# Kernel tuning notes

Measured on AMD Instinct MI355X. Metric: run time of the kernel, lower is better.

The kernel has to match this reference:

```python
import jax, jax.numpy as jnp
import numpy as np

B, N, H, E = 64, 512, 32, 4
N_STEPS = 5
ANNO = 1


def setup_inputs() -> dict:
    key = jax.random.key(0)
    ks = jax.random.split(key, 20)
    sc_h = 1.0 / np.sqrt(H)
    sc_3h = 1.0 / np.sqrt(3 * H)
    sc_ha = 1.0 / np.sqrt(H + ANNO)
    inp = {
        "x": jax.random.normal(ks[0], (B, N, H), jnp.float32),
        "a": jax.random.uniform(ks[1], (B, N, ANNO), jnp.float32),
        "m": jax.random.uniform(ks[2], (B, N, 2 * N * E), jnp.float32),
        # fc_in / fc_out: hidden -> hidden*n_edge (torch Linear: W [out,in])
        "W_in": jax.random.normal(ks[3], (H * E, H), jnp.float32) * sc_h,
        "b_in": jax.random.normal(ks[4], (H * E,), jnp.float32) * sc_h,
        "W_out": jax.random.normal(ks[5], (H * E, H), jnp.float32) * sc_h,
        "b_out": jax.random.normal(ks[6], (H * E,), jnp.float32) * sc_h,
        # GRU-style gates: 3*hidden -> hidden
        "Wz": jax.random.normal(ks[7], (H, 3 * H), jnp.float32) * sc_3h,
        "bz": jax.random.normal(ks[8], (H,), jnp.float32) * sc_3h,
        "Wr": jax.random.normal(ks[9], (H, 3 * H), jnp.float32) * sc_3h,
        "br": jax.random.normal(ks[10], (H,), jnp.float32) * sc_3h,
        "Wt": jax.random.normal(ks[11], (H, 3 * H), jnp.float32) * sc_3h,
        "bt": jax.random.normal(ks[12], (H,), jnp.float32) * sc_3h,
        # output head (task_id not in {18,19}): fc1, fc2
        "W1": jax.random.normal(ks[13], (H, H + ANNO), jnp.float32) * sc_ha,
        "b1": jax.random.normal(ks[14], (H,), jnp.float32) * sc_ha,
        "W2": jax.random.normal(ks[15], (1, H), jnp.float32) * sc_h,
        "b2": jax.random.normal(ks[16], (1,), jnp.float32) * sc_h,
    }
    return inp


def _reorder(s):
    # [B, N, H*E] -> view(B,N,H,E) -> transpose(2,3) -> transpose(1,2) -> [B, E*N, H]
    return s.reshape(B, N, H, E).transpose(0, 3, 1, 2).reshape(B, E * N, H)


def reference(x, a, m, W_in, b_in, W_out, b_out, Wz, bz, Wr, br, Wt, bt, W1, b1, W2, b2):
    m_in = m[:, :, : N * E]   # [B, N, N*E]
    m_out = m[:, :, N * E :]  # [B, N, N*E]
    h = x
    for _ in range(N_STEPS):
        s_in = _reorder(h @ W_in.T + b_in)    # [B, E*N, H]
        s_out = _reorder(h @ W_out.T + b_out)  # [B, E*N, H]
        a_in = jnp.einsum("bnm,bmh->bnh", m_in, s_in)
        a_out = jnp.einsum("bnm,bmh->bnh", m_out, s_out)
        cat = jnp.concatenate([a_in, a_out, h], axis=-1)  # [B, N, 3H]
        z = jax.nn.sigmoid(cat @ Wz.T + bz)
        r = jax.nn.sigmoid(cat @ Wr.T + br)
        joint = jnp.concatenate([a_in, a_out, r * h], axis=-1)
        h_hat = jnp.tanh(joint @ Wt.T + bt)
        h = (1.0 - z) * h + z * h_hat
    out = jnp.tanh(jnp.concatenate([h, a], axis=-1) @ W1.T + b1)  # [B, N, H]
    out = (out @ W2.T + b2).sum(-1)  # [B, N]
    return out
```

## Files before the change

### kernel.cpp

```cpp
#include <hip/hip_runtime.h>
#include <hip/hip_fp16.h>
#include <math.h>

#define B_ 64
#define N_ 512
#define H_ 32
#define E_ 4
#define NSTEPS 5
#define KTOT 2048

typedef _Float16 half8 __attribute__((ext_vector_type(8)));
typedef float   f32x4 __attribute__((ext_vector_type(4)));

__device__ __forceinline__ void gld16(const void* g, void* l) {
    __builtin_amdgcn_global_load_lds(
        (const __attribute__((address_space(1))) void*)g,
        (__attribute__((address_space(3))) void*)l, 16, 0, 0);
}

__global__ __launch_bounds__(256) void k_init_h(const float* __restrict__ x,
                                                float* __restrict__ h) {
    int i = blockIdx.x * blockDim.x + threadIdx.x;
    ((f32x4*)h)[i] = ((const f32x4*)x)[i];
}

__global__ __launch_bounds__(256) void k_s(const float* __restrict__ hstate,
                                           const float* __restrict__ W_in,
                                           const float* __restrict__ b_in,
                                           const float* __restrict__ W_out,
                                           const float* __restrict__ b_out,
                                           _Float16* __restrict__ sT_in_hi,
                                           _Float16* __restrict__ sT_in_lo,
                                           _Float16* __restrict__ sT_out_hi,
                                           _Float16* __restrict__ sT_out_lo) {
    int b  = blockIdx.x >> 3;
    int n0 = (blockIdx.x & 7) * 64;
    int lane = threadIdx.x & 63;
    int w = __builtin_amdgcn_readfirstlane((int)(threadIdx.x >> 6));
    int n = n0 + lane;

    const float* hrow = hstate + ((size_t)b * N_ + n) * H_;
    f32x4 hv[8];
#pragma unroll
    for (int c = 0; c < 8; c++) hv[c] = ((const f32x4*)hrow)[c];

#pragma unroll 4
    for (int o = 0; o < 32; o++) {
        int he = w * 32 + o;
        const f32x4* wr = (const f32x4*)(W_in + (size_t)he * H_);
        float acc = b_in[he];
#pragma unroll
        for (int c = 0; c < 8; c++) {
            f32x4 wv = wr[c];
            acc += hv[c][0]*wv[0] + hv[c][1]*wv[1] + hv[c][2]*wv[2] + hv[c][3]*wv[3];
        }
        int hh = he >> 2, e = he & 3;
        size_t idx = ((size_t)b * H_ + hh) * KTOT + e * N_ + n;
        _Float16 hi = (_Float16)acc;
        sT_in_hi[idx] = hi;
        sT_in_lo[idx] = (_Float16)(acc - (float)hi);
    }
#pragma unroll 4
    for (int o = 0; o < 32; o++) {
        int he = w * 32 + o;
        const f32x4* wr = (const f32x4*)(W_out + (size_t)he * H_);
        float acc = b_out[he];
#pragma unroll
        for (int c = 0; c < 8; c++) {
            f32x4 wv = wr[c];
            acc += hv[c][0]*wv[0] + hv[c][1]*wv[1] + hv[c][2]*wv[2] + hv[c][3]*wv[3];
        }
        int hh = he >> 2, e = he & 3;
        size_t idx = ((size_t)b * H_ + hh) * KTOT + e * N_ + n;
        _Float16 hi = (_Float16)acc;
        sT_out_hi[idx] = hi;
        sT_out_lo[idx] = (_Float16)(acc - (float)hi);
    }
}

#define BUFA 32768
#define BUFB 16384
__global__ __launch_bounds__(256) void k_einsum_gl(const float* __restrict__ m,
                                                   const _Float16* __restrict__ sT_in_hi,
                                                   const _Float16* __restrict__ sT_in_lo,
                                                   const _Float16* __restrict__ sT_out_hi,
                                                   const _Float16* __restrict__ sT_out_lo,
                                                   float* __restrict__ a_in,
                                                   float* __restrict__ a_out) {
    __shared__ __align__(16) char lds[2 * BUFA + 2 * BUFB];
    int nblk = blockIdx.x;
    int b    = blockIdx.y;
    int dir  = blockIdx.z;
    int n0   = nblk * 64;
    int tid  = threadIdx.x;
    int w    = tid >> 6;
    int lane = tid & 63;
    int l15  = lane & 15;
    int quad = lane >> 4;

    const char* mBase = (const char*)(m + ((size_t)(b * N_ + n0)) * (2 * KTOT)
                                        + (size_t)dir * KTOT);
    const _Float16* sHi = (dir ? sT_out_hi : sT_in_hi) + (size_t)b * H_ * KTOT;
    const _Float16* sLo = (dir ? sT_out_lo : sT_in_lo) + (size_t)b * H_ * KTOT;
    float* aout = dir ? a_out : a_in;

    int bp  = w >> 1;
    int brb = (w & 1) << 4;
    const _Float16* sP = bp ? sLo : sHi;

    auto STAGE = [&](int c, int buf) {
        char* dA = lds + buf * BUFA;
        char* dB = lds + 2 * BUFA + buf * BUFB + bp * 8192;
#pragma unroll
        for (int i = 0; i < 8; i++) {
            int r = (w << 4) + 2 * i + (lane >> 5);
            const char* g = mBase + (size_t)r * (2 * KTOT * 4) + c * 512
                            + (((lane & 31) * 16) ^ ((r & 7) << 4));
            gld16(g, dA + ((w << 4) + 2 * i) * 512);
        }
#pragma unroll
        for (int i = 0; i < 4; i++) {
            int r = brb + 4 * i + (lane >> 4);
            const char* g = (const char*)(sP + (size_t)r * KTOT) + c * 256
                            + (((lane & 15) * 16) ^ ((r & 7) << 4));
            gld16(g, dB + (brb + 4 * i) * 256);
        }
    };

    f32x4 acc0 = {0.f,0.f,0.f,0.f}, acc1 = {0.f,0.f,0.f,0.f};

    int rowA  = (w << 4) + l15;
    int swzA  = (rowA & 7) << 4;
    int swzB0 = (l15 & 7) << 4;

    STAGE(0, 0);
    __syncthreads();

    for (int c = 0; c < 16; c++) {
        int buf = c & 1;
        if (c < 15) STAGE(c + 1, buf ^ 1);

        const char* Ab = lds + buf * BUFA + rowA * 512;
        const char* Bh = lds + 2 * BUFA + buf * BUFB;
        const char* Bl = Bh + 8192;
#pragma unroll
        for (int it = 0; it < 4; it++) {
            int kab = it * 128 + quad * 32;
            f32x4 a0 = *(const f32x4*)(Ab + (kab ^ swzA));
            f32x4 a1 = *(const f32x4*)(Ab + ((kab + 16) ^ swzA));

            int kbb = it * 64 + quad * 16;
            int o0 = l15 * 256        + (kbb ^ swzB0);
            int o1 = (l15 + 16) * 256 + (kbb ^ swzB0);
            half8 Bhi0 = *(const half8*)(Bh + o0);
            half8 Bhi1 = *(const half8*)(Bh + o1);
            half8 Blo0 = *(const half8*)(Bl + o0);
            half8 Blo1 = *(const half8*)(Bl + o1);

            half8 Ahi, Alo;
#pragma unroll
            for (int j = 0; j < 4; j++) {
                float v0 = a0[j], v1 = a1[j];
                _Float16 h0 = (_Float16)v0, h1 = (_Float16)v1;
                Ahi[j]     = h0;
                Ahi[j + 4] = h1;
                Alo[j]     = (_Float16)(v0 - (float)h0);
                Alo[j + 4] = (_Float16)(v1 - (float)h1);
            }
            acc0 = __builtin_amdgcn_mfma_f32_16x16x32_f16(Ahi, Bhi0, acc0, 0, 0, 0);
            acc1 = __builtin_amdgcn_mfma_f32_16x16x32_f16(Ahi, Bhi1, acc1, 0, 0, 0);
            acc0 = __builtin_amdgcn_mfma_f32_16x16x32_f16(Ahi, Blo0, acc0, 0, 0, 0);
            acc1 = __builtin_amdgcn_mfma_f32_16x16x32_f16(Ahi, Blo1, acc1, 0, 0, 0);
            acc0 = __builtin_amdgcn_mfma_f32_16x16x32_f16(Alo, Bhi0, acc0, 0, 0, 0);
            acc1 = __builtin_amdgcn_mfma_f32_16x16x32_f16(Alo, Bhi1, acc1, 0, 0, 0);
        }
        __syncthreads();
    }

#pragma unroll
    for (int r = 0; r < 4; r++) {
        size_t rr = (size_t)b * N_ + (n0 + w * 16 + quad * 4 + r);
        aout[rr * H_ + l15]      = acc0[r];
        aout[rr * H_ + 16 + l15] = acc1[r];
    }
}

__global__ __launch_bounds__(256) void k_gate(const float* __restrict__ a_in,
                                              const float* __restrict__ a_out,
                                              float* __restrict__ hstate,
                                              const float* __restrict__ Wz,
                                              const float* __restrict__ bz,
                                              const float* __restrict__ Wr,
                                              const float* __restrict__ br,
                                              const float* __restrict__ Wt,
                                              const float* __restrict__ bt) {
    __shared__ float cat[8][96];
    __shared__ float rh[8][32];
    int base = blockIdx.x * 8;
    int t = threadIdx.x;

    for (int idx = t; idx < 768; idx += 256) {
        int r = idx / 96, c = idx - r * 96;
        size_t row = (size_t)(base + r);
        float v;
        if (c < 32)      v = a_in [row * 32 + c];
        else if (c < 64) v = a_out[row * 32 + (c - 32)];
        else             v = hstate[row * 32 + (c - 64)];
        cat[r][c] = v;
    }
    __syncthreads();

    int r = t >> 5, i = t & 31;
    float az = bz[i], ar = br[i];
    const f32x4* wzr = (const f32x4*)(Wz + (size_t)i * 96);
    const f32x4* wrr = (const f32x4*)(Wr + (size_t)i * 96);
    const f32x4* crow = (const f32x4*)cat[r];
#pragma unroll
    for (int kc = 0; kc < 24; kc++) {
        f32x4 cv = crow[kc];
        f32x4 wz = wzr[kc];
        f32x4 wr = wrr[kc];
        az += cv[0]*wz[0] + cv[1]*wz[1] + cv[2]*wz[2] + cv[3]*wz[3];
        ar += cv[0]*wr[0] + cv[1]*wr[1] + cv[2]*wr[2] + cv[3]*wr[3];
    }
    float z  = 1.f / (1.f + __expf(-az));
    float rg = 1.f / (1.f + __expf(-ar));
    float hold = cat[r][64 + i];
    rh[r][i] = rg * hold;
    __syncthreads();

    float at = bt[i];
    const f32x4* wtr = (const f32x4*)(Wt + (size_t)i * 96);
#pragma unroll
    for (int kc = 0; kc < 16; kc++) {
        f32x4 cv = crow[kc];
        f32x4 wt = wtr[kc];
        at += cv[0]*wt[0] + cv[1]*wt[1] + cv[2]*wt[2] + cv[3]*wt[3];
    }
    const f32x4* rrow = (const f32x4*)rh[r];
#pragma unroll
    for (int kc = 0; kc < 8; kc++) {
        f32x4 cv = rrow[kc];
        f32x4 wt = wtr[16 + kc];
        at += cv[0]*wt[0] + cv[1]*wt[1] + cv[2]*wt[2] + cv[3]*wt[3];
    }
    float hh = tanhf(at);
    hstate[(size_t)(base + r) * 32 + i] = (1.f - z) * hold + z * hh;
}

__global__ __launch_bounds__(256) void k_final(const float* __restrict__ hstate,
                                               const float* __restrict__ a,
                                               const float* __restrict__ W1,
                                               const float* __restrict__ b1,
                                               const float* __restrict__ W2,
                                               const float* __restrict__ b2,
                                               float* __restrict__ out) {
    __shared__ float hl[8][32];
    __shared__ float as[8];
    int base = blockIdx.x * 8;
    int t = threadIdx.x;
    {
        int r = t >> 5, c = t & 31;
        hl[r][c] = hstate[(size_t)(base + r) * 32 + c];
        if (t < 8) as[t] = a[base + t];
    }
    __syncthreads();
    int r = t >> 5, j = t & 31;
    float acc = b1[j];
    const float* w1r = W1 + (size_t)j * 33;
#pragma unroll
    for (int i2 = 0; i2 < 32; i2++) acc += hl[r][i2] * w1r[i2];
    acc += as[r] * w1r[32];
    float o = tanhf(acc) * W2[j];
#pragma unroll
    for (int off = 16; off; off >>= 1) o += __shfl_xor(o, off, 32);
    if (j == 0) out[base + r] = o + b2[0];
}

extern "C" void kernel_launch(void* const* d_in, const int* in_sizes, int n_in,
                              void* d_out, int out_size, void* d_ws, size_t ws_size,
                              hipStream_t stream) {
    const float* x     = (const float*)d_in[0];
    const float* a     = (const float*)d_in[1];
    const float* m     = (const float*)d_in[2];
    const float* W_in  = (const float*)d_in[3];
    const float* b_in  = (const float*)d_in[4];
    const float* W_out = (const float*)d_in[5];
    const float* b_out = (const float*)d_in[6];
    const float* Wz    = (const float*)d_in[7];
    const float* bz    = (const float*)d_in[8];
    const float* Wr    = (const float*)d_in[9];
    const float* br    = (const float*)d_in[10];
    const float* Wt    = (const float*)d_in[11];
    const float* bt    = (const float*)d_in[12];
    const float* W1    = (const float*)d_in[13];
    const float* b1    = (const float*)d_in[14];
    const float* W2    = (const float*)d_in[15];
    const float* b2    = (const float*)d_in[16];
    float* out = (float*)d_out;

    char* ws = (char*)d_ws;
    float*    h         = (float*)(ws);
    float*    a_in      = (float*)(ws + ((size_t)4  << 20));
    float*    a_out     = (float*)(ws + ((size_t)8  << 20));
    _Float16* sT_in_hi  = (_Float16*)(ws + ((size_t)12 << 20));
    _Float16* sT_in_lo  = (_Float16*)(ws + ((size_t)20 << 20));
    _Float16* sT_out_hi = (_Float16*)(ws + ((size_t)28 << 20));
    _Float16* sT_out_lo = (_Float16*)(ws + ((size_t)36 << 20));

    k_init_h<<<1024, 256, 0, stream>>>(x, h);
    for (int s = 0; s < NSTEPS; s++) {
        k_s<<<512, 256, 0, stream>>>(h, W_in, b_in, W_out, b_out,
                                     sT_in_hi, sT_in_lo, sT_out_hi, sT_out_lo);
        k_einsum_gl<<<dim3(8, 64, 2), 256, 0, stream>>>(m, sT_in_hi, sT_in_lo,
                                                        sT_out_hi, sT_out_lo,
                                                        a_in, a_out);
        k_gate<<<4096, 256, 0, stream>>>(a_in, a_out, h, Wz, bz, Wr, br, Wt, bt);
    }
    k_final<<<4096, 256, 0, stream>>>(h, a, W1, b1, W2, b2, out);
}
```

Measured before the change: 2.183 ms.

## Triple-buffer einsum K-chunks with explicit vmcnt waits and XCD-aware block mapping

Rewrites the batched einsum kernel to use half-size K chunks (32 chunks instead of 16) staged through a 3-deep LDS ring with two chunks in flight. Explicit s_waitcnt vmcnt counts and raw s_barrier replace __syncthreads. The kernel asks for 2 blocks per CU via launch bounds, cutting LDS to 72KB. The grid is flattened and remapped so the blocks of one (batch, direction) pair land on the same XCD, aiming for L2 reuse of the shared s matrix. This hides more global-load latency behind the MFMAs, at the cost of more barriers per K, and correctness depends on the hand-counted vmcnt values.

```diff
diff --git a/kernel.cpp b/kernel.cpp
--- a/kernel.cpp
+++ b/kernel.cpp
@@ -78,19 +78,25 @@
     }
 }
 
-#define BUFA 32768
-#define BUFB 16384
-__global__ __launch_bounds__(256) void k_einsum_gl(const float* __restrict__ m,
-                                                   const _Float16* __restrict__ sT_in_hi,
-                                                   const _Float16* __restrict__ sT_in_lo,
-                                                   const _Float16* __restrict__ sT_out_hi,
-                                                   const _Float16* __restrict__ sT_out_lo,
-                                                   float* __restrict__ a_in,
-                                                   float* __restrict__ a_out) {
-    __shared__ __align__(16) char lds[2 * BUFA + 2 * BUFB];
-    int nblk = blockIdx.x;
-    int b    = blockIdx.y;
-    int dir  = blockIdx.z;
+#define CHB   256
+#define BUFA2 16384
+#define BUFB2 8192
+#define BUFSZ 24576
+#define NCH   32
+__global__ __launch_bounds__(256, 2) void k_einsum_p3(const float* __restrict__ m,
+                                                      const _Float16* __restrict__ sT_in_hi,
+                                                      const _Float16* __restrict__ sT_in_lo,
+                                                      const _Float16* __restrict__ sT_out_hi,
+                                                      const _Float16* __restrict__ sT_out_lo,
+                                                      float* __restrict__ a_in,
+                                                      float* __restrict__ a_out) {
+    __shared__ __align__(16) char lds[3 * BUFSZ];
+    int bid  = blockIdx.x;
+    int xcd  = bid & 7, loc = bid >> 3;
+    int pair = xcd * 16 + (loc >> 3);
+    int nblk = loc & 7;
+    int b    = pair >> 1;
+    int dir  = pair & 1;
     int n0   = nblk * 64;
     int tid  = threadIdx.x;
     int w    = tid >> 6;
@@ -104,26 +110,26 @@
     const _Float16* sLo = (dir ? sT_out_lo : sT_in_lo) + (size_t)b * H_ * KTOT;
     float* aout = dir ? a_out : a_in;
 
-    int bp  = w >> 1;
-    int brb = (w & 1) << 4;
-    const _Float16* sP = bp ? sLo : sHi;
+    int bp   = w >> 1;
+    int brb  = (w & 1) << 4;
+    const char* sP = (const char*)(bp ? sLo : sHi);
 
     auto STAGE = [&](int c, int buf) {
-        char* dA = lds + buf * BUFA;
-        char* dB = lds + 2 * BUFA + buf * BUFB + bp * 8192;
-#pragma unroll
-        for (int i = 0; i < 8; i++) {
-            int r = (w << 4) + 2 * i + (lane >> 5);
-            const char* g = mBase + (size_t)r * (2 * KTOT * 4) + c * 512
-                            + (((lane & 31) * 16) ^ ((r & 7) << 4));
-            gld16(g, dA + ((w << 4) + 2 * i) * 512);
-        }
+        char* dA = lds + buf * BUFSZ;
+        char* dB = lds + buf * BUFSZ + BUFA2 + bp * 4096;
 #pragma unroll
         for (int i = 0; i < 4; i++) {
-            int r = brb + 4 * i + (lane >> 4);
-            const char* g = (const char*)(sP + (size_t)r * KTOT) + c * 256
+            int r = (w << 4) + i * 4 + (lane >> 4);
+            const char* g = mBase + (size_t)r * (2 * KTOT * 4) + c * CHB
                             + (((lane & 15) * 16) ^ ((r & 7) << 4));
-            gld16(g, dB + (brb + 4 * i) * 256);
+            gld16(g, dA + ((w << 4) + i * 4) * 256);
+        }
+#pragma unroll
+        for (int i = 0; i < 2; i++) {
+            int r = brb + i * 8 + (lane >> 3);
+            const char* g = sP + (size_t)r * (KTOT * 2) + c * 128
+                            + (((lane & 7) * 16) ^ ((r & 7) << 4));
+            gld16(g, dB + (brb + i * 8) * 128);
         }
     };
 
@@ -134,24 +140,29 @@
     int swzB0 = (l15 & 7) << 4;
 
     STAGE(0, 0);
-    __syncthreads();
-
-    for (int c = 0; c < 16; c++) {
-        int buf = c & 1;
-        if (c < 15) STAGE(c + 1, buf ^ 1);
-
-        const char* Ab = lds + buf * BUFA + rowA * 512;
-        const char* Bh = lds + 2 * BUFA + buf * BUFB;
-        const char* Bl = Bh + 8192;
-#pragma unroll
-        for (int it = 0; it < 4; it++) {
+    STAGE(1, 1);
+
+    for (int c = 0; c < NCH; c++) {
+        int buf = c % 3;
+        if (c + 2 < NCH) STAGE(c + 2, (c + 2) % 3);
+        if (c + 2 < NCH)      asm volatile("s_waitcnt vmcnt(12)" ::: "memory");
+        else if (c + 1 < NCH) asm volatile("s_waitcnt vmcnt(6)"  ::: "memory");
+        else                  asm volatile("s_waitcnt vmcnt(0)"  ::: "memory");
+        __builtin_amdgcn_s_barrier();
+        __builtin_amdgcn_sched_barrier(0);
+
+        const char* Ab = lds + buf * BUFSZ + rowA * 256;
+        const char* Bh = lds + buf * BUFSZ + BUFA2;
+        const char* Bl = Bh + 4096;
+#pragma unroll
+        for (int it = 0; it < 2; it++) {
             int kab = it * 128 + quad * 32;
             f32x4 a0 = *(const f32x4*)(Ab + (kab ^ swzA));
             f32x4 a1 = *(const f32x4*)(Ab + ((kab + 16) ^ swzA));
 
             int kbb = it * 64 + quad * 16;
-            int o0 = l15 * 256        + (kbb ^ swzB0);
-            int o1 = (l15 + 16) * 256 + (kbb ^ swzB0);
+            int o0 = l15 * 128        + (kbb ^ swzB0);
+            int o1 = (l15 + 16) * 128 + (kbb ^ swzB0);
             half8 Bhi0 = *(const half8*)(Bh + o0);
             half8 Bhi1 = *(const half8*)(Bh + o1);
             half8 Blo0 = *(const half8*)(Bl + o0);
@@ -174,7 +185,8 @@
             acc0 = __builtin_amdgcn_mfma_f32_16x16x32_f16(Alo, Bhi0, acc0, 0, 0, 0);
             acc1 = __builtin_amdgcn_mfma_f32_16x16x32_f16(Alo, Bhi1, acc1, 0, 0, 0);
         }
-        __syncthreads();
+        __builtin_amdgcn_sched_barrier(0);
+        __builtin_amdgcn_s_barrier();
     }
 
 #pragma unroll
@@ -312,9 +324,9 @@
     for (int s = 0; s < NSTEPS; s++) {
         k_s<<<512, 256, 0, stream>>>(h, W_in, b_in, W_out, b_out,
                                      sT_in_hi, sT_in_lo, sT_out_hi, sT_out_lo);
-        k_einsum_gl<<<dim3(8, 64, 2), 256, 0, stream>>>(m, sT_in_hi, sT_in_lo,
-                                                        sT_out_hi, sT_out_lo,
-                                                        a_in, a_out);
+        k_einsum_p3<<<1024, 256, 0, stream>>>(m, sT_in_hi, sT_in_lo,
+                                              sT_out_hi, sT_out_lo,
+                                              a_in, a_out);
         k_gate<<<4096, 256, 0, stream>>>(a_in, a_out, h, Wz, bz, Wr, br, Wt, bt);
     }
     k_final<<<4096, 256, 0, stream>>>(h, a, W1, b1, W2, b2, out);
```

Result: no change. 2.176 ms (-0.3%).

## Fuse s projection into einsum kernel, recomputing s tiles in LDS per K-chunk

Applied to the files above, without the earlier changes.

Removes the separate k_s kernel and its hi/lo fp16 intermediate buffers. Each einsum block now stages h rows into LDS, computes the W_in/W_out projection for the current K-chunk, splits it into hi/lo fp16 directly in LDS, then runs the MFMAs. The K-chunk is halved (32 iterations) with explicit vmcnt waits and raw barriers, and the h copy kernel is dropped by reading x directly on step 0. The price is redundant projection compute across the 8 n-blocks per batch and extra barriers per chunk.

```diff
diff --git a/kernel.cpp b/kernel.cpp
--- a/kernel.cpp
+++ b/kernel.cpp
@@ -18,76 +18,18 @@
         (__attribute__((address_space(3))) void*)l, 16, 0, 0);
 }
 
-__global__ __launch_bounds__(256) void k_init_h(const float* __restrict__ x,
-                                                float* __restrict__ h) {
-    int i = blockIdx.x * blockDim.x + threadIdx.x;
-    ((f32x4*)h)[i] = ((const f32x4*)x)[i];
-}
-
-__global__ __launch_bounds__(256) void k_s(const float* __restrict__ hstate,
-                                           const float* __restrict__ W_in,
-                                           const float* __restrict__ b_in,
-                                           const float* __restrict__ W_out,
-                                           const float* __restrict__ b_out,
-                                           _Float16* __restrict__ sT_in_hi,
-                                           _Float16* __restrict__ sT_in_lo,
-                                           _Float16* __restrict__ sT_out_hi,
-                                           _Float16* __restrict__ sT_out_lo) {
-    int b  = blockIdx.x >> 3;
-    int n0 = (blockIdx.x & 7) * 64;
-    int lane = threadIdx.x & 63;
-    int w = __builtin_amdgcn_readfirstlane((int)(threadIdx.x >> 6));
-    int n = n0 + lane;
-
-    const float* hrow = hstate + ((size_t)b * N_ + n) * H_;
-    f32x4 hv[8];
-#pragma unroll
-    for (int c = 0; c < 8; c++) hv[c] = ((const f32x4*)hrow)[c];
-
-#pragma unroll 4
-    for (int o = 0; o < 32; o++) {
-        int he = w * 32 + o;
-        const f32x4* wr = (const f32x4*)(W_in + (size_t)he * H_);
-        float acc = b_in[he];
-#pragma unroll
-        for (int c = 0; c < 8; c++) {
-            f32x4 wv = wr[c];
-            acc += hv[c][0]*wv[0] + hv[c][1]*wv[1] + hv[c][2]*wv[2] + hv[c][3]*wv[3];
-        }
-        int hh = he >> 2, e = he & 3;
-        size_t idx = ((size_t)b * H_ + hh) * KTOT + e * N_ + n;
-        _Float16 hi = (_Float16)acc;
-        sT_in_hi[idx] = hi;
-        sT_in_lo[idx] = (_Float16)(acc - (float)hi);
-    }
-#pragma unroll 4
-    for (int o = 0; o < 32; o++) {
-        int he = w * 32 + o;
-        const f32x4* wr = (const f32x4*)(W_out + (size_t)he * H_);
-        float acc = b_out[he];
-#pragma unroll
-        for (int c = 0; c < 8; c++) {
-            f32x4 wv = wr[c];
-            acc += hv[c][0]*wv[0] + hv[c][1]*wv[1] + hv[c][2]*wv[2] + hv[c][3]*wv[3];
-        }
-        int hh = he >> 2, e = he & 3;
-        size_t idx = ((size_t)b * H_ + hh) * KTOT + e * N_ + n;
-        _Float16 hi = (_Float16)acc;
-        sT_out_hi[idx] = hi;
-        sT_out_lo[idx] = (_Float16)(acc - (float)hi);
-    }
-}
-
-#define BUFA 32768
-#define BUFB 16384
-__global__ __launch_bounds__(256) void k_einsum_gl(const float* __restrict__ m,
-                                                   const _Float16* __restrict__ sT_in_hi,
-                                                   const _Float16* __restrict__ sT_in_lo,
-                                                   const _Float16* __restrict__ sT_out_hi,
-                                                   const _Float16* __restrict__ sT_out_lo,
-                                                   float* __restrict__ a_in,
-                                                   float* __restrict__ a_out) {
-    __shared__ __align__(16) char lds[2 * BUFA + 2 * BUFB];
+#define ABUF 16384
+#define HBUF 8192
+#define BBUF 8192
+__global__ __launch_bounds__(256) void k_es(const float* __restrict__ m,
+                                            const float* __restrict__ hsrc,
+                                            const float* __restrict__ W_in,
+                                            const float* __restrict__ b_in,
+                                            const float* __restrict__ W_out,
+                                            const float* __restrict__ b_out,
+                                            float* __restrict__ a_in,
+                                            float* __restrict__ a_out) {
+    __shared__ __align__(16) char lds[2 * ABUF + 2 * HBUF + 2 * BBUF];
     int nblk = blockIdx.x;
     int b    = blockIdx.y;
     int dir  = blockIdx.z;
@@ -97,33 +39,32 @@
     int lane = tid & 63;
     int l15  = lane & 15;
     int quad = lane >> 4;
+    int hu   = __builtin_amdgcn_readfirstlane(tid >> 6);
 
     const char* mBase = (const char*)(m + ((size_t)(b * N_ + n0)) * (2 * KTOT)
                                         + (size_t)dir * KTOT);
-    const _Float16* sHi = (dir ? sT_out_hi : sT_in_hi) + (size_t)b * H_ * KTOT;
-    const _Float16* sLo = (dir ? sT_out_lo : sT_in_lo) + (size_t)b * H_ * KTOT;
+    const char* hB = (const char*)(hsrc + (size_t)b * N_ * H_);
+    const float* Wf  = dir ? W_out : W_in;
+    const float* bfp = dir ? b_out : b_in;
     float* aout = dir ? a_out : a_in;
 
-    int bp  = w >> 1;
-    int brb = (w & 1) << 4;
-    const _Float16* sP = bp ? sLo : sHi;
-
     auto STAGE = [&](int c, int buf) {
-        char* dA = lds + buf * BUFA;
-        char* dB = lds + 2 * BUFA + buf * BUFB + bp * 8192;
-#pragma unroll
-        for (int i = 0; i < 8; i++) {
-            int r = (w << 4) + 2 * i + (lane >> 5);
-            const char* g = mBase + (size_t)r * (2 * KTOT * 4) + c * 512
-                            + (((lane & 31) * 16) ^ ((r & 7) << 4));
-            gld16(g, dA + ((w << 4) + 2 * i) * 512);
-        }
+        char* dA = lds + buf * ABUF;
+        char* dH = lds + 2 * ABUF + buf * HBUF;
 #pragma unroll
         for (int i = 0; i < 4; i++) {
-            int r = brb + 4 * i + (lane >> 4);
-            const char* g = (const char*)(sP + (size_t)r * KTOT) + c * 256
+            int r = (w << 4) + i * 4 + (lane >> 4);
+            const char* g = mBase + (size_t)r * (2 * KTOT * 4) + c * 256
                             + (((lane & 15) * 16) ^ ((r & 7) << 4));
-            gld16(g, dB + (brb + 4 * i) * 256);
+            gld16(g, dA + ((w << 4) + i * 4) * 256);
+        }
+        int hrow0 = (c & 7) * 64;
+#pragma unroll
+        for (int i = 0; i < 2; i++) {
+            int rl = lane >> 3, pp = lane & 7;
+            const char* g = hB + (size_t)(hrow0 + w * 16 + i * 8 + rl) * 128
+                            + ((pp ^ (rl & 7)) * 16);
+            gld16(g, dH + w * 2048 + i * 1024);
         }
     };
 
@@ -134,24 +75,61 @@
     int swzB0 = (l15 & 7) << 4;
 
     STAGE(0, 0);
-    __syncthreads();
-
-    for (int c = 0; c < 16; c++) {
+
+    for (int c = 0; c < 32; c++) {
         int buf = c & 1;
-        if (c < 15) STAGE(c + 1, buf ^ 1);
-
-        const char* Ab = lds + buf * BUFA + rowA * 512;
-        const char* Bh = lds + 2 * BUFA + buf * BUFB;
-        const char* Bl = Bh + 8192;
-#pragma unroll
-        for (int it = 0; it < 4; it++) {
+        if (c < 31) STAGE(c + 1, buf ^ 1);
+        if (c < 31) asm volatile("s_waitcnt vmcnt(6)" ::: "memory");
+        else        asm volatile("s_waitcnt vmcnt(0)" ::: "memory");
+        __builtin_amdgcn_s_barrier();
+        __builtin_amdgcn_sched_barrier(0);
+
+        char* Bb = lds + 2 * ABUF + 2 * HBUF + buf * BBUF;
+
+        {
+            const char* hC = lds + 2 * ABUF + buf * HBUF;
+            int j = lane;
+            f32x4 hv[8];
+#pragma unroll
+            for (int u = 0; u < 8; u++)
+                hv[u] = *(const f32x4*)(hC + j * 128 + ((u ^ (j & 7)) * 16));
+            int e = c >> 3;
+#pragma unroll
+            for (int i = 0; i < 8; i++) {
+                int hr = hu * 8 + i;
+                int he = hr * 4 + e;
+                const f32x4* wr = (const f32x4*)(Wf + (size_t)he * H_);
+                float acc = bfp[he];
+#pragma unroll
+                for (int c8 = 0; c8 < 8; c8++) {
+                    f32x4 wv = wr[c8];
+                    acc += hv[c8][0]*wv[0] + hv[c8][1]*wv[1]
+                         + hv[c8][2]*wv[2] + hv[c8][3]*wv[3];
+                }
+                _Float16 hi = (_Float16)acc;
+                _Float16 lo = (_Float16)(acc - (float)hi);
+                int byte = hr * 128 + ((j * 2) ^ ((hr & 7) << 4));
+                *(_Float16*)(Bb + byte)        = hi;
+                *(_Float16*)(Bb + 4096 + byte) = lo;
+            }
+        }
+        asm volatile("s_waitcnt lgkmcnt(0)" ::: "memory");
+        __builtin_amdgcn_sched_barrier(0);
+        __builtin_amdgcn_s_barrier();
+        __builtin_amdgcn_sched_barrier(0);
+
+        const char* Ab = lds + buf * ABUF + rowA * 256;
+        const char* Bh = Bb;
+        const char* Bl = Bb + 4096;
+#pragma unroll
+        for (int it = 0; it < 2; it++) {
             int kab = it * 128 + quad * 32;
             f32x4 a0 = *(const f32x4*)(Ab + (kab ^ swzA));
             f32x4 a1 = *(const f32x4*)(Ab + ((kab + 16) ^ swzA));
 
             int kbb = it * 64 + quad * 16;
-            int o0 = l15 * 256        + (kbb ^ swzB0);
-            int o1 = (l15 + 16) * 256 + (kbb ^ swzB0);
+            int o0 = l15 * 128        + (kbb ^ swzB0);
+            int o1 = (l15 + 16) * 128 + (kbb ^ swzB0);
             half8 Bhi0 = *(const half8*)(Bh + o0);
             half8 Bhi1 = *(const half8*)(Bh + o1);
             half8 Blo0 = *(const half8*)(Bl + o0);
@@ -159,13 +137,13 @@
 
             half8 Ahi, Alo;
 #pragma unroll
-            for (int j = 0; j < 4; j++) {
-                float v0 = a0[j], v1 = a1[j];
+            for (int jj = 0; jj < 4; jj++) {
+                float v0 = a0[jj], v1 = a1[jj];
                 _Float16 h0 = (_Float16)v0, h1 = (_Float16)v1;
-                Ahi[j]     = h0;
-                Ahi[j + 4] = h1;
-                Alo[j]     = (_Float16)(v0 - (float)h0);
-                Alo[j + 4] = (_Float16)(v1 - (float)h1);
+                Ahi[jj]     = h0;
+                Ahi[jj + 4] = h1;
+                Alo[jj]     = (_Float16)(v0 - (float)h0);
+                Alo[jj + 4] = (_Float16)(v1 - (float)h1);
             }
             acc0 = __builtin_amdgcn_mfma_f32_16x16x32_f16(Ahi, Bhi0, acc0, 0, 0, 0);
             acc1 = __builtin_amdgcn_mfma_f32_16x16x32_f16(Ahi, Bhi1, acc1, 0, 0, 0);
@@ -174,7 +152,6 @@
             acc0 = __builtin_amdgcn_mfma_f32_16x16x32_f16(Alo, Bhi0, acc0, 0, 0, 0);
             acc1 = __builtin_amdgcn_mfma_f32_16x16x32_f16(Alo, Bhi1, acc1, 0, 0, 0);
         }
-        __syncthreads();
     }
 
 #pragma unroll
@@ -187,6 +164,7 @@
 
 __global__ __launch_bounds__(256) void k_gate(const float* __restrict__ a_in,
                                               const float* __restrict__ a_out,
+                                              const float* __restrict__ hold_src,
                                               float* __restrict__ hstate,
                                               const float* __restrict__ Wz,
                                               const float* __restrict__ bz,
@@ -205,7 +183,7 @@
         float v;
         if (c < 32)      v = a_in [row * 32 + c];
         else if (c < 64) v = a_out[row * 32 + (c - 32)];
-        else             v = hstate[row * 32 + (c - 64)];
+        else             v = hold_src[row * 32 + (c - 64)];
         cat[r][c] = v;
     }
     __syncthreads();
@@ -300,22 +278,16 @@
     float* out = (float*)d_out;
 
     char* ws = (char*)d_ws;
-    float*    h         = (float*)(ws);
-    float*    a_in      = (float*)(ws + ((size_t)4  << 20));
-    float*    a_out     = (float*)(ws + ((size_t)8  << 20));
-    _Float16* sT_in_hi  = (_Float16*)(ws + ((size_t)12 << 20));
-    _Float16* sT_in_lo  = (_Float16*)(ws + ((size_t)20 << 20));
-    _Float16* sT_out_hi = (_Float16*)(ws + ((size_t)28 << 20));
-    _Float16* sT_out_lo = (_Float16*)(ws + ((size_t)36 << 20));
-
-    k_init_h<<<1024, 256, 0, stream>>>(x, h);
+    float* h    = (float*)(ws);
+    float* a_in = (float*)(ws + ((size_t)4 << 20));
+    float* a_out= (float*)(ws + ((size_t)8 << 20));
+
     for (int s = 0; s < NSTEPS; s++) {
-        k_s<<<512, 256, 0, stream>>>(h, W_in, b_in, W_out, b_out,
-                                     sT_in_hi, sT_in_lo, sT_out_hi, sT_out_lo);
-        k_einsum_gl<<<dim3(8, 64, 2), 256, 0, stream>>>(m, sT_in_hi, sT_in_lo,
-                                                        sT_out_hi, sT_out_lo,
-                                                        a_in, a_out);
-        k_gate<<<4096, 256, 0, stream>>>(a_in, a_out, h, Wz, bz, Wr, br, Wt, bt);
+        const float* hsrc = (s == 0) ? x : h;
+        k_es<<<dim3(8, 64, 2), 256, 0, stream>>>(m, hsrc, W_in, b_in,
+                                                 W_out, b_out, a_in, a_out);
+        k_gate<<<4096, 256, 0, stream>>>(a_in, a_out, hsrc, h,
+                                         Wz, bz, Wr, br, Wt, bt);
     }
     k_final<<<4096, 256, 0, stream>>>(h, a, W1, b1, W2, b2, out);
 }
```

Result: no change. 2.188 ms (+0.2%).
